# Kernel optimization log

Measured on AMD Instinct MI355X. Metric: run time of the kernel, lower is better.

The kernel has to match this reference:

```python
import jax, jax.numpy as jnp
import numpy as np

M, K, N = 8192, 4096, 4096

def _quantize_symmetric(t):
    # per-tensor symmetric int8 quantization: scale = max|t| / 127
    scale = jnp.max(jnp.abs(t)) / 127.0
    q = jnp.clip(jnp.round(t / scale), -127.0, 127.0).astype(jnp.int8)
    return q, scale


def setup_inputs() -> dict:
    key = jax.random.key(0)
    kx, kw, kb = jax.random.split(key, 3)
    x = jax.random.normal(kx, (M, K), dtype=jnp.float32)
    weight = jax.random.normal(kw, (N, K), dtype=jnp.float32)
    bias = jax.random.normal(kb, (N,), dtype=jnp.float32)
    return {"x": x, "weight": weight, "bias": bias}


def reference(x, weight, bias):
    # dynamic per-tensor quantization of activations and (pre-quantized) weight
    x_q, x_scale = _quantize_symmetric(x)
    w_q, w_scale = _quantize_symmetric(weight)
    # int8 GEMM with int32 accumulation (padding in the source is a no-op mathematically)
    acc = jnp.matmul(x_q.astype(jnp.int32), w_q.astype(jnp.int32).T)  # [M, N]
    # dequantize with product of per-tensor scales, then bias add
    out = acc.astype(jnp.float32) * (x_scale * w_scale) + bias
    return out
```

## Files before the change

### kernel.cpp

```cpp
#include <hip/hip_runtime.h>
#include <stdint.h>

#define MDIM 8192
#define KDIM 4096
#define NDIM 4096

typedef int v4i __attribute__((ext_vector_type(4)));

__global__ __launch_bounds__(256) void absmax2_kernel(const float* __restrict__ x,
                                                      const float* __restrict__ w,
                                                      unsigned* __restrict__ bits) {
    __shared__ float smax[4];
    const float4* src;
    int idx, stride, n4;
    unsigned* slot;
    if (blockIdx.x < 1024) {
        src = (const float4*)x;
        idx = blockIdx.x * 256 + threadIdx.x;
        stride = 1024 * 256;
        n4 = MDIM * KDIM / 4;
        slot = bits;
    } else {
        src = (const float4*)w;
        idx = (blockIdx.x - 1024) * 256 + threadIdx.x;
        stride = 512 * 256;
        n4 = NDIM * KDIM / 4;
        slot = bits + 1;
    }
    float m = 0.0f;
    for (int i = idx; i < n4; i += 4 * stride) {
        float4 a = src[i];
        float4 b = src[i + stride];
        float4 c = src[i + 2 * stride];
        float4 d = src[i + 3 * stride];
        m = fmaxf(m, fmaxf(fmaxf(fabsf(a.x), fabsf(a.y)), fmaxf(fabsf(a.z), fabsf(a.w))));
        m = fmaxf(m, fmaxf(fmaxf(fabsf(b.x), fabsf(b.y)), fmaxf(fabsf(b.z), fabsf(b.w))));
        m = fmaxf(m, fmaxf(fmaxf(fabsf(c.x), fabsf(c.y)), fmaxf(fabsf(c.z), fabsf(c.w))));
        m = fmaxf(m, fmaxf(fmaxf(fabsf(d.x), fabsf(d.y)), fmaxf(fabsf(d.z), fabsf(d.w))));
    }
#pragma unroll
    for (int off = 32; off > 0; off >>= 1)
        m = fmaxf(m, __shfl_down(m, off, 64));
    if ((threadIdx.x & 63) == 0) smax[threadIdx.x >> 6] = m;
    __syncthreads();
    if (threadIdx.x == 0) {
        float bm = fmaxf(fmaxf(smax[0], smax[1]), fmaxf(smax[2], smax[3]));
        atomicMax(slot, __float_as_uint(bm));
    }
}

__global__ __launch_bounds__(256) void quant2_kernel(const float* __restrict__ x,
                                                     const float* __restrict__ w,
                                                     const unsigned* __restrict__ bits,
                                                     int* __restrict__ xq,
                                                     int* __restrict__ wq) {
    const float4* src;
    int idx, stride, n4;
    int* dst;
    float amax;
    if (blockIdx.x < 2048) {
        src = (const float4*)x;
        idx = blockIdx.x * 256 + threadIdx.x;
        stride = 2048 * 256;
        n4 = MDIM * KDIM / 4;
        dst = xq;
        amax = __uint_as_float(bits[0]);
    } else {
        src = (const float4*)w;
        idx = (blockIdx.x - 2048) * 256 + threadIdx.x;
        stride = 1024 * 256;
        n4 = NDIM * KDIM / 4;
        dst = wq;
        amax = __uint_as_float(bits[1]);
    }
    const float scale = (amax > 0.0f) ? (amax / 127.0f) : 1.0f;
    for (int i = idx; i < n4; i += 4 * stride) {
        float4 v[4];
        v[0] = src[i];
        v[1] = src[i + stride];
        v[2] = src[i + 2 * stride];
        v[3] = src[i + 3 * stride];
#pragma unroll
        for (int u = 0; u < 4; ++u) {
            int a = __float2int_rn(v[u].x / scale);
            int b = __float2int_rn(v[u].y / scale);
            int c = __float2int_rn(v[u].z / scale);
            int d = __float2int_rn(v[u].w / scale);
            a = min(127, max(-127, a));
            b = min(127, max(-127, b));
            c = min(127, max(-127, c));
            d = min(127, max(-127, d));
            dst[i + u * stride] =
                (a & 0xFF) | ((b & 0xFF) << 8) | ((c & 0xFF) << 16) | ((d & 0xFF) << 24);
        }
    }
}

__global__ __launch_bounds__(512, 2) void gemm_i8(
    const signed char* __restrict__ Aq,
    const signed char* __restrict__ Wq,
    const float* __restrict__ bias,
    const unsigned* __restrict__ bits,
    float* __restrict__ out) {
    __shared__ __align__(16) signed char As[2 * 32768];
    __shared__ __align__(16) signed char Bs[2 * 32768];

    const int tid  = threadIdx.x;
    const int lane = tid & 63;
    const int wave = tid >> 6;
    const int wm = wave >> 2;
    const int wn = wave & 3;
    const int l15 = lane & 15;
    const int l4  = lane >> 4;
    const int swz = l15 & 7;

    const int m0 = blockIdx.y * 256;
    const int n0 = blockIdx.x * 256;

    const int srow = tid >> 3;
    const int scol = ((tid & 7) ^ (srow & 7)) << 4;
    const signed char* aSrc[4];
    const signed char* bSrc[4];
#pragma unroll
    for (int c = 0; c < 4; ++c) {
        aSrc[c] = Aq + (size_t)(m0 + c * 64 + srow) * KDIM + scol;
        bSrc[c] = Wq + (size_t)(n0 + c * 64 + srow) * KDIM + scol;
    }
    const int ldst = tid * 16;

    v4i acc[8][4] = {};
    v4i af[4][2], bf[4][2];

#define GLL(SRC, DST) __builtin_amdgcn_global_load_lds(                                   \
        (const __attribute__((address_space(1))) void*)(SRC),                             \
        (__attribute__((address_space(3))) void*)(DST), 16, 0, 0)

#define STG_A(BUF, h, KO) do {                                                            \
    GLL(aSrc[(h)*2 + 0] + (KO), As + (BUF)*32768 + (h)*16384 + 0*8192 + ldst);            \
    GLL(aSrc[(h)*2 + 1] + (KO), As + (BUF)*32768 + (h)*16384 + 1*8192 + ldst);            \
} while (0)
#define STG_B(BUF, h, KO) do {                                                            \
    GLL(bSrc[(h)*2 + 0] + (KO), Bs + (BUF)*32768 + (h)*16384 + 0*8192 + ldst);            \
    GLL(bSrc[(h)*2 + 1] + (KO), Bs + (BUF)*32768 + (h)*16384 + 1*8192 + ldst);            \
} while (0)

#define LDA(BUF, i, kk) (*(const v4i*)(As + (BUF)*32768 +                                 \
        (wm*128 + (i)*16 + l15)*128 + (((((kk)<<2) | l4) ^ swz) << 4)))
#define LDB(BUF, j, kk) (*(const v4i*)(Bs + (BUF)*32768 +                                 \
        (wn*64 + (j)*16 + l15)*128 + (((((kk)<<2) | l4) ^ swz) << 4)))

#define MQ(I0, J0) do {                                                                   \
    _Pragma("unroll") for (int kk = 0; kk < 2; ++kk)                                      \
    _Pragma("unroll") for (int i = 0; i < 4; ++i)                                         \
    _Pragma("unroll") for (int j = 0; j < 2; ++j)                                         \
        acc[(I0)+i][(J0)+j] = __builtin_amdgcn_mfma_i32_16x16x64_i8(                      \
            af[i][kk], bf[(J0)+j][kk], acc[(I0)+i][(J0)+j], 0, 0, 0);                     \
} while (0)

#define BAR()   do { __builtin_amdgcn_s_barrier(); asm volatile("" ::: "memory"); } while (0)
#define LGKM0() asm volatile("s_waitcnt lgkmcnt(0)" ::: "memory")
#define VMC(n)  asm volatile("s_waitcnt vmcnt(" #n ")" ::: "memory")

#define TILE_BODY(BUF, NBUF, KO1, KO2, ST_Q0, ST_Q123, VMQ3) do {                         \
                       \
    _Pragma("unroll") for (int j = 0; j < 2; ++j) {                                       \
        bf[j][0] = LDB(BUF, j, 0); bf[j][1] = LDB(BUF, j, 1); }                           \
    _Pragma("unroll") for (int i = 0; i < 4; ++i) {                                       \
        af[i][0] = LDA(BUF, i, 0); af[i][1] = LDA(BUF, i, 1); }                           \
    if (ST_Q0) STG_A(NBUF, 1, KO1);                                                       \
    BAR(); LGKM0();                                                                       \
    __builtin_amdgcn_s_setprio(1); MQ(0, 0); __builtin_amdgcn_s_setprio(0);               \
    BAR();                                                                                \
                                     \
    _Pragma("unroll") for (int j = 0; j < 2; ++j) {                                       \
        bf[2+j][0] = LDB(BUF, 2+j, 0); bf[2+j][1] = LDB(BUF, 2+j, 1); }                   \
    if (ST_Q123) STG_B(BUF, 0, KO2);                                                      \
    BAR(); LGKM0();                                                                       \
    __builtin_amdgcn_s_setprio(1); MQ(0, 2); __builtin_amdgcn_s_setprio(0);               \
    BAR();                                                                                \
                 \
    _Pragma("unroll") for (int i = 0; i < 4; ++i) {                                       \
        af[i][0] = LDA(BUF, 4+i, 0); af[i][1] = LDA(BUF, 4+i, 1); }                       \
    if (ST_Q123) STG_B(BUF, 1, KO2);                                                      \
    BAR(); LGKM0();                                                                       \
    __builtin_amdgcn_s_setprio(1); MQ(4, 0); __builtin_amdgcn_s_setprio(0);               \
    BAR();                                                                                \
                            \
    if (ST_Q123) STG_A(BUF, 0, KO2);                                                      \
    BAR();                                                                                \
    __builtin_amdgcn_s_setprio(1); MQ(4, 2); __builtin_amdgcn_s_setprio(0);               \
    VMQ3;                                                                                 \
    BAR();                                                                                \
} while (0)

    STG_B(0, 0, 0); STG_B(0, 1, 0); STG_A(0, 0, 0); STG_A(0, 1, 0);
    STG_B(1, 0, 128); STG_B(1, 1, 128); STG_A(1, 0, 128);
    VMC(6);
    BAR();

#pragma unroll 1
    for (int kt = 0; kt < 15; ++kt) {
        const int kb = kt * 256;
        TILE_BODY(0, 1, kb + 128, kb + 256, 1, 1, VMC(6));
        TILE_BODY(1, 0, kb + 256, kb + 384, 1, 1, VMC(6));
    }
    TILE_BODY(0, 1, 3968, 0, 1, 0, VMC(0));
    TILE_BODY(1, 0, 0, 0, 0, 0, ((void)0));

    const float ax = __uint_as_float(bits[0]);
    const float aw = __uint_as_float(bits[1]);
    const float s = (ax / 127.0f) * (aw / 127.0f);

#pragma unroll
    for (int j = 0; j < 4; ++j) {
        const int col = n0 + wn * 64 + j * 16 + l15;
        const float bcol = bias[col];
#pragma unroll
        for (int i = 0; i < 8; ++i) {
            const int row0 = m0 + wm * 128 + i * 16 + l4 * 4;
#pragma unroll
            for (int r = 0; r < 4; ++r)
                out[(size_t)(row0 + r) * NDIM + col] = (float)acc[i][j][r] * s + bcol;
        }
    }
#undef GLL
#undef STG_A
#undef STG_B
#undef LDA
#undef LDB
#undef MQ
#undef BAR
#undef LGKM0
#undef VMC
#undef TILE_BODY
}

extern "C" void kernel_launch(void* const* d_in, const int* in_sizes, int n_in,
                              void* d_out, int out_size, void* d_ws, size_t ws_size,
                              hipStream_t stream) {
    const float* x    = (const float*)d_in[0];
    const float* w    = (const float*)d_in[1];
    const float* bias = (const float*)d_in[2];
    float* out = (float*)d_out;

    unsigned* bits = (unsigned*)d_ws;
    signed char* xq = (signed char*)d_ws + 64;
    signed char* wq = xq + (size_t)MDIM * KDIM;

    hipMemsetAsync(d_ws, 0, 64, stream);

    absmax2_kernel<<<1536, 256, 0, stream>>>(x, w, bits);
    quant2_kernel<<<3072, 256, 0, stream>>>(x, w, bits, (int*)xq, (int*)wq);

    dim3 grid(NDIM / 256, MDIM / 256);
    gemm_i8<<<grid, 512, 0, stream>>>(xq, wq, bias, bits, out);
}
```

Before: 454.9 us.

## Reorder int8 GEMM pipeline to prefetch next tile fragments and remap block order

The int8 MFMA main loop is rescheduled. B fragments and the first half of the A fragments for the next K tile are now read from LDS at the end of the current tile. The remaining A fragments are read between MFMA quadrants. The quadrant order changes to (0,0),(0,2),(4,2),(4,0), which cuts the number of barriers and LDS-wait stalls per tile. The block index is also remapped so that consecutive workgroups are spread over row and column tiles, which is meant to improve L2/MALL reuse. This risks more register pressure from holding all four B fragments, and a tighter vmcnt wait that could be wrong if the count of outstanding loads does not match.

```diff
diff --git a/kernel.cpp b/kernel.cpp
--- a/kernel.cpp
+++ b/kernel.cpp
@@ -114,8 +114,10 @@
     const int l4  = lane >> 4;
     const int swz = l15 & 7;
 
-    const int m0 = blockIdx.y * 256;
-    const int n0 = blockIdx.x * 256;
+    const int lin = blockIdx.y * gridDim.x + blockIdx.x;
+    const int nl  = (lin & 7) * 64 + (lin >> 3);
+    const int m0 = (nl >> 4) * 256;
+    const int n0 = (nl & 15) * 256;
 
     const int srow = tid >> 3;
     const int scol = ((tid & 7) ^ (srow & 7)) << 4;
@@ -161,35 +163,38 @@
 #define LGKM0() asm volatile("s_waitcnt lgkmcnt(0)" ::: "memory")
 #define VMC(n)  asm volatile("s_waitcnt vmcnt(" #n ")" ::: "memory")
 
-#define TILE_BODY(BUF, NBUF, KO1, KO2, ST_Q0, ST_Q123, VMQ3) do {                         \
-                       \
-    _Pragma("unroll") for (int j = 0; j < 2; ++j) {                                       \
+#define RD_AFH(BUF) do {                                                                  \
+    _Pragma("unroll") for (int i = 0; i < 4; ++i) {                                       \
+        af[i][0] = LDA(BUF, 4 + i, 0); af[i][1] = LDA(BUF, 4 + i, 1); }                   \
+} while (0)
+#define RD_BOUND(BUF) do {                                                                \
+    _Pragma("unroll") for (int j = 0; j < 4; ++j) {                                       \
         bf[j][0] = LDB(BUF, j, 0); bf[j][1] = LDB(BUF, j, 1); }                           \
     _Pragma("unroll") for (int i = 0; i < 4; ++i) {                                       \
         af[i][0] = LDA(BUF, i, 0); af[i][1] = LDA(BUF, i, 1); }                           \
-    if (ST_Q0) STG_A(NBUF, 1, KO1);                                                       \
-    BAR(); LGKM0();                                                                       \
+} while (0)
+
+#define TILE_BODY(BUF, NBUF, KO1, KO2, ST0, ST123, VMQ2, DO_BOUND) do {                   \
+                                                               \
+    if (ST0) STG_A(NBUF, 1, KO1);                                                         \
+    LGKM0();                                                                              \
     __builtin_amdgcn_s_setprio(1); MQ(0, 0); __builtin_amdgcn_s_setprio(0);               \
     BAR();                                                                                \
-                                     \
-    _Pragma("unroll") for (int j = 0; j < 2; ++j) {                                       \
-        bf[2+j][0] = LDB(BUF, 2+j, 0); bf[2+j][1] = LDB(BUF, 2+j, 1); }                   \
-    if (ST_Q123) STG_B(BUF, 0, KO2);                                                      \
-    BAR(); LGKM0();                                                                       \
+                                              \
+    if (ST123) STG_B(BUF, 0, KO2);                                                        \
     __builtin_amdgcn_s_setprio(1); MQ(0, 2); __builtin_amdgcn_s_setprio(0);               \
-    BAR();                                                                                \
-                 \
-    _Pragma("unroll") for (int i = 0; i < 4; ++i) {                                       \
-        af[i][0] = LDA(BUF, 4+i, 0); af[i][1] = LDA(BUF, 4+i, 1); }                       \
-    if (ST_Q123) STG_B(BUF, 1, KO2);                                                      \
-    BAR(); LGKM0();                                                                       \
+    RD_AFH(BUF);                                                                          \
+    BAR();                                                                                \
+                                      \
+    if (ST123) STG_B(BUF, 1, KO2);                                                        \
+    LGKM0();                                                                              \
+    __builtin_amdgcn_s_setprio(1); MQ(4, 2); __builtin_amdgcn_s_setprio(0);               \
+    VMQ2;                                                                                 \
+    BAR();                                                                                \
+                       \
+    if (ST123) STG_A(BUF, 0, KO2);                                                        \
     __builtin_amdgcn_s_setprio(1); MQ(4, 0); __builtin_amdgcn_s_setprio(0);               \
-    BAR();                                                                                \
-                            \
-    if (ST_Q123) STG_A(BUF, 0, KO2);                                                      \
-    BAR();                                                                                \
-    __builtin_amdgcn_s_setprio(1); MQ(4, 2); __builtin_amdgcn_s_setprio(0);               \
-    VMQ3;                                                                                 \
+    if (DO_BOUND) RD_BOUND(NBUF);                                                         \
     BAR();                                                                                \
 } while (0)
 
@@ -197,15 +202,16 @@
     STG_B(1, 0, 128); STG_B(1, 1, 128); STG_A(1, 0, 128);
     VMC(6);
     BAR();
+    RD_BOUND(0);
 
 #pragma unroll 1
     for (int kt = 0; kt < 15; ++kt) {
         const int kb = kt * 256;
-        TILE_BODY(0, 1, kb + 128, kb + 256, 1, 1, VMC(6));
-        TILE_BODY(1, 0, kb + 256, kb + 384, 1, 1, VMC(6));
-    }
-    TILE_BODY(0, 1, 3968, 0, 1, 0, VMC(0));
-    TILE_BODY(1, 0, 0, 0, 0, 0, ((void)0));
+        TILE_BODY(0, 1, kb + 128, kb + 256, 1, 1, VMC(4), 1);
+        TILE_BODY(1, 0, kb + 256, kb + 384, 1, 1, VMC(4), 1);
+    }
+    TILE_BODY(0, 1, 3968, 0, 1, 0, VMC(0), 1);
+    TILE_BODY(1, 0, 0, 0, 0, 0, ((void)0), 0);
 
     const float ax = __uint_as_float(bits[0]);
     const float aw = __uint_as_float(bits[1]);
@@ -232,6 +238,8 @@
 #undef BAR
 #undef LGKM0
 #undef VMC
+#undef RD_AFH
+#undef RD_BOUND
 #undef TILE_BODY
 }
 
```

Measured after the change: 442.7 us. 1.03x faster.
